# Kernel optimization log

Hardware: AMD Instinct MI355X
Metric: run time of the kernel (lower is better)

## Reference

```python
import jax, jax.numpy as jnp
from jax import lax
import numpy as np

INPUT_SIZE = 128
T = 64
B = 8192
HIDDENS = [32, 16, 8]
FUTURE = 1


def _lstm_layer(x, w_ih, w_hh, b_ih, b_hh):
    """PyTorch-semantics single-layer LSTM, batch_first, zero init state.
    x: [B,T,D]; w_ih: [4H,D]; w_hh: [4H,H]; b_ih,b_hh: [4H]. Gate order i,f,g,o.
    Returns all hidden states [B,T,H]."""
    Bsz = x.shape[0]
    H = w_hh.shape[1]
    # Precompute input contribution for all timesteps in one big GEMM.
    xg = jnp.einsum('btd,gd->btg', x, w_ih) + b_ih + b_hh  # [B,T,4H]
    xg_t = jnp.swapaxes(xg, 0, 1)  # [T,B,4H]

    def step(carry, xt):
        h, c = carry
        gates = xt + h @ w_hh.T  # [B,4H]
        i, f, g, o = jnp.split(gates, 4, axis=-1)
        i = jax.nn.sigmoid(i)
        f = jax.nn.sigmoid(f)
        g = jnp.tanh(g)
        o = jax.nn.sigmoid(o)
        c = f * c + i * g
        h = o * jnp.tanh(c)
        return (h, c), h

    init = (jnp.zeros((Bsz, H), x.dtype), jnp.zeros((Bsz, H), x.dtype))
    _, hs = lax.scan(step, init, xg_t)  # hs: [T,B,H]
    return jnp.swapaxes(hs, 0, 1)


def setup_inputs() -> dict:
    key = jax.random.key(0)
    ks = jax.random.split(key, 16)
    s = 0.1

    def rn(k, shape):
        return jax.random.normal(k, shape, dtype=jnp.float32) * s

    inp = {
        'x': jax.random.normal(ks[0], (B, T, INPUT_SIZE), dtype=jnp.float32),
        'w_ih1': rn(ks[1], (4 * 32, INPUT_SIZE)),
        'w_hh1': rn(ks[2], (4 * 32, 32)),
        'b_ih1': rn(ks[3], (4 * 32,)),
        'b_hh1': rn(ks[4], (4 * 32,)),
        'w_ih2': rn(ks[5], (4 * 16, 32)),
        'w_hh2': rn(ks[6], (4 * 16, 16)),
        'b_ih2': rn(ks[7], (4 * 16,)),
        'b_hh2': rn(ks[8], (4 * 16,)),
        'w_ih3': rn(ks[9], (4 * 8, 16)),
        'w_hh3': rn(ks[10], (4 * 8, 8)),
        'b_ih3': rn(ks[11], (4 * 8,)),
        'b_hh3': rn(ks[12], (4 * 8,)),
        'fc_w': rn(ks[13], (FUTURE, 8)),
        'fc_b': rn(ks[14], (FUTURE,)),
    }
    return inp


def reference(x, w_ih1, w_hh1, b_ih1, b_hh1, w_ih2, w_hh2, b_ih2, b_hh2,
              w_ih3, w_hh3, b_ih3, b_hh3, fc_w, fc_b):
    h = _lstm_layer(x, w_ih1, w_hh1, b_ih1, b_hh1)   # [B,T,32]
    h = _lstm_layer(h, w_ih2, w_hh2, b_ih2, b_hh2)   # [B,T,16]
    h = _lstm_layer(h, w_ih3, w_hh3, b_ih3, b_hh3)   # [B,T,8]
    return h[:, -1, :] @ fc_w.T + fc_b               # [B, FUTURE]
```

## Files before the change

### kernel.cpp

```cpp
#include <hip/hip_runtime.h>
#include <cstddef>
#include <type_traits>


typedef _Float16 h8_t  __attribute__((ext_vector_type(8)));
typedef __fp16   p2_t  __attribute__((ext_vector_type(2)));
typedef float    f4_t  __attribute__((ext_vector_type(4)));

#define T_LEN 64
#define D_IN  128

__device__ __forceinline__ float sig_(float x)  { return 1.0f / (1.0f + __expf(-x)); }
__device__ __forceinline__ float tanh_(float x) { float e = __expf(2.0f * x); return 1.0f - 2.0f / (e + 1.0f); }

__device__ __forceinline__ h8_t zero8h() {
    h8_t r = { (_Float16)0.f,(_Float16)0.f,(_Float16)0.f,(_Float16)0.f,
               (_Float16)0.f,(_Float16)0.f,(_Float16)0.f,(_Float16)0.f };
    return r;
}
__device__ __forceinline__ h8_t cvt8(f4_t lo, f4_t hi) {
    union { h8_t v8; p2_t v2[4]; } u;
    u.v2[0] = __builtin_amdgcn_cvt_pkrtz(lo[0], lo[1]);
    u.v2[1] = __builtin_amdgcn_cvt_pkrtz(lo[2], lo[3]);
    u.v2[2] = __builtin_amdgcn_cvt_pkrtz(hi[0], hi[1]);
    u.v2[3] = __builtin_amdgcn_cvt_pkrtz(hi[2], hi[3]);
    return u.v8;
}
__device__ __forceinline__ h8_t load8f_h(const float* __restrict__ p) {
    f4_t lo = *(const f4_t*)p, hi = *(const f4_t*)(p + 4);
    return cvt8(lo, hi);
}

__global__ __launch_bounds__(256, 2)
void lstm_one(const float* __restrict__ x,
              const float* __restrict__ w_ih1, const float* __restrict__ w_hh1,
              const float* __restrict__ b_ih1, const float* __restrict__ b_hh1,
              const float* __restrict__ w_ih2, const float* __restrict__ w_hh2,
              const float* __restrict__ b_ih2, const float* __restrict__ b_hh2,
              const float* __restrict__ w_ih3, const float* __restrict__ w_hh3,
              const float* __restrict__ b_ih3, const float* __restrict__ b_hh3,
              const float* __restrict__ fc_w, const float* __restrict__ fc_b,
              float* __restrict__ out)
{
    __shared__ __align__(16) _Float16 h1s[2][16][40];
    __shared__ __align__(16) _Float16 h2s[2][16][24];
    __shared__ __align__(16) _Float16 h3s[2][16][8];
    __shared__ __align__(16) _Float16 xs[2][16 * 128];

    const int tid  = threadIdx.x;
    const int lane = tid & 63;
    const int wid  = tid >> 6;
    const int nl = lane & 15, qd = lane >> 4;
    const int n7 = nl & 7;
    const bool lo8 = (nl & 8) == 0;

    h8_t bw1[2][4], bh1[2];
    #pragma unroll
    for (int j = 0; j < 2; ++j) {
        int G = 8 * wid + n7 + 32 * ((nl >> 3) + 2 * j);
        #pragma unroll
        for (int kc = 0; kc < 4; ++kc)
            bw1[j][kc] = load8f_h(w_ih1 + G * 128 + kc * 32 + qd * 8);
        bh1[j] = load8f_h(w_hh1 + G * 32 + qd * 8);
    }
    h8_t bw2[2] = {zero8h(), zero8h()}, bh2[2] = {zero8h(), zero8h()};
    float bs2[4] = {0.f, 0.f, 0.f, 0.f};
    if (wid < 2) {
        #pragma unroll
        for (int j = 0; j < 2; ++j) {
            int G = 32 * j + 16 * (nl >> 3) + 8 * wid + n7;
            bw2[j] = load8f_h(w_ih2 + G * 32 + qd * 8);
            bh2[j] = (qd < 2) ? load8f_h(w_hh2 + G * 16 + qd * 8) : zero8h();
        }
        int u2 = 8 * wid + n7;
        #pragma unroll
        for (int g = 0; g < 4; ++g) bs2[g] = b_ih2[16 * g + u2] + b_hh2[16 * g + u2];
    }
    h8_t b3c[2] = {zero8h(), zero8h()};
    float bs3[4] = {0.f, 0.f, 0.f, 0.f};
    if (wid >= 2) {
        #pragma unroll
        for (int j = 0; j < 2; ++j) {
            int G = 16 * j + 8 * (nl >> 3) + n7;
            b3c[j] = (qd < 2) ? load8f_h(w_ih3 + G * 16 + qd * 8)
                   : (qd == 2) ? load8f_h(w_hh3 + G * 8) : zero8h();
        }
        #pragma unroll
        for (int g = 0; g < 4; ++g) bs3[g] = b_ih3[8 * g + n7] + b_hh3[8 * g + n7];
    }
    float bs1[4];
    {
        int u1 = 8 * wid + n7;
        #pragma unroll
        for (int g = 0; g < 4; ++g) bs1[g] = b_ih1[32 * g + u1] + b_hh1[32 * g + u1];
    }

    for (int i = tid; i < 2 * 16 * 40; i += 256) (&h1s[0][0][0])[i] = (_Float16)0.f;
    for (int i = tid; i < 2 * 16 * 24; i += 256) (&h2s[0][0][0])[i] = (_Float16)0.f;
    for (int i = tid; i < 2 * 16 * 8;  i += 256) (&h3s[0][0][0])[i] = (_Float16)0.f;

    float c1[2] = {0.f, 0.f};
    float c2[2] = {0.f, 0.f};
    float c3    = 0.f;

    const int b0 = blockIdx.x * 16;

    const int xrow = tid >> 4, xcc = tid & 15;
    const float* xg = x + ((size_t)(b0 + xrow) * T_LEN) * D_IN + xcc * 8;
    const int xws = (xrow * 16 + (xcc ^ (xrow & 7))) * 8;

    f4_t xa0 = *(const f4_t*)xg, xa1 = *(const f4_t*)(xg + 4);
    *(h8_t*)&xs[0][xws] = cvt8(xa0, xa1);
    xa0 = *(const f4_t*)(xg + D_IN);
    xa1 = *(const f4_t*)(xg + D_IN + 4);
    __syncthreads();

    auto step = [&](auto d1c, auto d2c, auto d3c, auto pc, int t) {
        constexpr bool DO1 = decltype(d1c)::value;
        constexpr bool DO2 = decltype(d2c)::value;
        constexpr bool DO3 = decltype(d3c)::value;
        constexpr int  P   = decltype(pc)::value;

        h8_t a1p = zero8h();
        if constexpr (DO1 || DO2)
            a1p = *(const h8_t*)&h1s[1 - P][nl][qd * 8];

        if constexpr (DO1) {
            h8_t af[4];
            #pragma unroll
            for (int kc = 0; kc < 4; ++kc)
                af[kc] = *(const h8_t*)&xs[P][(nl * 16 + ((4 * kc + qd) ^ n7)) * 8];

            h8_t xcur = cvt8(xa0, xa1);
            {
                int tn = (t + 2 < T_LEN) ? (t + 2) : (T_LEN - 1);
                const float* xn = xg + (size_t)tn * D_IN;
                xa0 = *(const f4_t*)xn;
                xa1 = *(const f4_t*)(xn + 4);
            }
            *(h8_t*)&xs[1 - P][xws] = xcur;

            f4_t acc[2];
            #pragma unroll
            for (int j = 0; j < 2; ++j) {
                f4_t a_ = {0.f, 0.f, 0.f, 0.f};
                #pragma unroll
                for (int kc = 0; kc < 4; ++kc)
                    a_ = __builtin_amdgcn_mfma_f32_16x16x32_f16(af[kc], bw1[j][kc], a_, 0, 0, 0);
                a_ = __builtin_amdgcn_mfma_f32_16x16x32_f16(a1p, bh1[j], a_, 0, 0, 0);
                acc[j] = a_;
            }
            #pragma unroll
            for (int rr = 0; rr < 2; ++rr) {
                float s0 = lo8 ? acc[0][rr + 2] : acc[0][rr];
                float s1 = lo8 ? acc[1][rr + 2] : acc[1][rr];
                float x0 = __shfl_xor(s0, 8, 64);
                float x1 = __shfl_xor(s1, 8, 64);
                float vi = lo8 ? acc[0][rr] : x0;
                float vf = lo8 ? x0 : acc[0][rr + 2];
                float vg = lo8 ? acc[1][rr] : x1;
                float vo = lo8 ? x1 : acc[1][rr + 2];
                float ig = sig_(vi + bs1[0]);
                float fg = sig_(vf + bs1[1]);
                float gg = tanh_(vg + bs1[2]);
                float og = sig_(vo + bs1[3]);
                float c = fg * c1[rr] + ig * gg; c1[rr] = c;
                float h = og * tanh_(c);
                h1s[P][4 * qd + rr + (lo8 ? 0 : 2)][8 * wid + n7] = (_Float16)h;
            }
        }

        if constexpr (DO2) {
            if (wid < 2) {
                h8_t a2p = zero8h();
                if (qd < 2) a2p = *(const h8_t*)&h2s[P][nl][qd * 8];
                f4_t acc2[2];
                #pragma unroll
                for (int j = 0; j < 2; ++j) {
                    f4_t a_ = {0.f, 0.f, 0.f, 0.f};
                    a_ = __builtin_amdgcn_mfma_f32_16x16x32_f16(a1p, bw2[j], a_, 0, 0, 0);
                    a_ = __builtin_amdgcn_mfma_f32_16x16x32_f16(a2p, bh2[j], a_, 0, 0, 0);
                    acc2[j] = a_;
                }
                #pragma unroll
                for (int rr = 0; rr < 2; ++rr) {
                    float s0 = lo8 ? acc2[0][rr + 2] : acc2[0][rr];
                    float s1 = lo8 ? acc2[1][rr + 2] : acc2[1][rr];
                    float x0 = __shfl_xor(s0, 8, 64);
                    float x1 = __shfl_xor(s1, 8, 64);
                    float vi = lo8 ? acc2[0][rr] : x0;
                    float vf = lo8 ? x0 : acc2[0][rr + 2];
                    float vg = lo8 ? acc2[1][rr] : x1;
                    float vo = lo8 ? x1 : acc2[1][rr + 2];
                    float ig = sig_(vi + bs2[0]);
                    float fg = sig_(vf + bs2[1]);
                    float gg = tanh_(vg + bs2[2]);
                    float og = sig_(vo + bs2[3]);
                    float c = fg * c2[rr] + ig * gg; c2[rr] = c;
                    float h = og * tanh_(c);
                    h2s[1 - P][4 * qd + rr + (lo8 ? 0 : 2)][8 * wid + n7] = (_Float16)h;
                }
            }
        }

        if constexpr (DO3) {
            if (wid >= 2) {
                h8_t a3 = zero8h();
                if (qd < 2)       a3 = *(const h8_t*)&h2s[P][nl][qd * 8];
                else if (qd == 2) a3 = *(const h8_t*)&h3s[1 - P][nl][0];
                f4_t acc3[2];
                #pragma unroll
                for (int j = 0; j < 2; ++j) {
                    f4_t a_ = {0.f, 0.f, 0.f, 0.f};
                    acc3[j] = __builtin_amdgcn_mfma_f32_16x16x32_f16(a3, b3c[j], a_, 0, 0, 0);
                }
                auto l3c = [&](auto rpc) {
                    constexpr int rp = decltype(rpc)::value;
                    float eLo = acc3[0][rp], eHi = acc3[0][rp + 2];
                    float oLo = acc3[1][rp], oHi = acc3[1][rp + 2];
                    float se = lo8 ? eHi : eLo; float xe = __shfl_xor(se, 8, 64);
                    float so = lo8 ? oHi : oLo; float xo = __shfl_xor(so, 8, 64);
                    float vi = lo8 ? eLo : xe;
                    float vf = lo8 ? xe  : eHi;
                    float vg = lo8 ? oLo : xo;
                    float vo = lo8 ? xo  : oHi;
                    float ig = sig_(vi + bs3[0]);
                    float fg = sig_(vf + bs3[1]);
                    float gg = tanh_(vg + bs3[2]);
                    float og = sig_(vo + bs3[3]);
                    float c = fg * c3 + ig * gg; c3 = c;
                    float h = og * tanh_(c);
                    h3s[P][4 * qd + rp + (lo8 ? 0 : 2)][n7] = (_Float16)h;
                };
                if (wid == 2) l3c(std::integral_constant<int, 0>{});
                else          l3c(std::integral_constant<int, 1>{});
            }
        }

        __syncthreads();
    };

    using TT = std::integral_constant<bool, true>;
    using FF = std::integral_constant<bool, false>;
    using P0 = std::integral_constant<int, 0>;
    using P1 = std::integral_constant<int, 1>;

    step(TT{}, FF{}, FF{}, P0{}, 0);
    step(TT{}, TT{}, FF{}, P1{}, 1);
    for (int tb = 1; tb < 32; ++tb) {
        step(TT{}, TT{}, TT{}, P0{}, 2 * tb);
        step(TT{}, TT{}, TT{}, P1{}, 2 * tb + 1);
    }
    step(FF{}, TT{}, TT{}, P0{}, 64);
    step(FF{}, FF{}, TT{}, P1{}, 65);

    if (tid < 16) {
        float a = fc_b[0];
        #pragma unroll
        for (int u = 0; u < 8; ++u)
            a += fc_w[u] * (float)h3s[1][tid][u];
        out[b0 + tid] = a;
    }
}

extern "C" void kernel_launch(void* const* d_in, const int* in_sizes, int n_in,
                              void* d_out, int out_size, void* d_ws, size_t ws_size,
                              hipStream_t stream) {
    (void)in_sizes; (void)n_in; (void)out_size; (void)d_ws; (void)ws_size;
    const float* x     = (const float*)d_in[0];
    const float* w_ih1 = (const float*)d_in[1];
    const float* w_hh1 = (const float*)d_in[2];
    const float* b_ih1 = (const float*)d_in[3];
    const float* b_hh1 = (const float*)d_in[4];
    const float* w_ih2 = (const float*)d_in[5];
    const float* w_hh2 = (const float*)d_in[6];
    const float* b_ih2 = (const float*)d_in[7];
    const float* b_hh2 = (const float*)d_in[8];
    const float* w_ih3 = (const float*)d_in[9];
    const float* w_hh3 = (const float*)d_in[10];
    const float* b_ih3 = (const float*)d_in[11];
    const float* b_hh3 = (const float*)d_in[12];
    const float* fc_w  = (const float*)d_in[13];
    const float* fc_b  = (const float*)d_in[14];

    dim3 grid(512), block(256);
    hipLaunchKernelGGL(lstm_one, grid, block, 0, stream,
                       x, w_ih1, w_hh1, b_ih1, b_hh1,
                       w_ih2, w_hh2, b_ih2, b_hh2,
                       w_ih3, w_hh3, b_ih3, b_hh3,
                       fc_w, fc_b, (float*)d_out);
}
```

Baseline: 411.7 us.

## Double block to 512 threads, splitting LSTM elementwise rows across wave pairs

Launches 8 waves per block instead of 4. Each pair of waves redundantly runs the same MFMAs, but each wave handles only one of the two row halves in the gate nonlinearity, which halves the serial elementwise chain per wave. The x prefetch is now split into 4-float chunks per thread, and the per-step __syncthreads is replaced by an explicit lgkmcnt wait plus s_barrier. The cost is duplicated MFMA work and weight registers, and a barrier across more waves.

```diff
diff --git a/kernel.cpp b/kernel.cpp
--- a/kernel.cpp
+++ b/kernel.cpp
@@ -4,6 +4,7 @@
 
 
 typedef _Float16 h8_t  __attribute__((ext_vector_type(8)));
+typedef _Float16 h4_t  __attribute__((ext_vector_type(4)));
 typedef __fp16   p2_t  __attribute__((ext_vector_type(2)));
 typedef float    f4_t  __attribute__((ext_vector_type(4)));
 
@@ -26,12 +27,23 @@
     u.v2[3] = __builtin_amdgcn_cvt_pkrtz(hi[2], hi[3]);
     return u.v8;
 }
+__device__ __forceinline__ h4_t cvt4(f4_t v) {
+    union { h4_t v4; p2_t v2[2]; } u;
+    u.v2[0] = __builtin_amdgcn_cvt_pkrtz(v[0], v[1]);
+    u.v2[1] = __builtin_amdgcn_cvt_pkrtz(v[2], v[3]);
+    return u.v4;
+}
 __device__ __forceinline__ h8_t load8f_h(const float* __restrict__ p) {
     f4_t lo = *(const f4_t*)p, hi = *(const f4_t*)(p + 4);
     return cvt8(lo, hi);
 }
 
-__global__ __launch_bounds__(256, 2)
+__device__ __forceinline__ void bar_lds() {
+    asm volatile("s_waitcnt lgkmcnt(0)" ::: "memory");
+    __builtin_amdgcn_s_barrier();
+}
+
+__global__ __launch_bounds__(512, 4)
 void lstm_one(const float* __restrict__ x,
               const float* __restrict__ w_ih1, const float* __restrict__ w_hh1,
               const float* __restrict__ b_ih1, const float* __restrict__ b_hh1,
@@ -49,7 +61,9 @@
 
     const int tid  = threadIdx.x;
     const int lane = tid & 63;
-    const int wid  = tid >> 6;
+    const int wid8 = tid >> 6;
+    const int w    = wid8 & 3;
+    const int rsel = wid8 >> 2;
     const int nl = lane & 15, qd = lane >> 4;
     const int n7 = nl & 7;
     const bool lo8 = (nl & 8) == 0;
@@ -57,7 +71,7 @@
     h8_t bw1[2][4], bh1[2];
     #pragma unroll
     for (int j = 0; j < 2; ++j) {
-        int G = 8 * wid + n7 + 32 * ((nl >> 3) + 2 * j);
+        int G = 8 * w + n7 + 32 * ((nl >> 3) + 2 * j);
         #pragma unroll
         for (int kc = 0; kc < 4; ++kc)
             bw1[j][kc] = load8f_h(w_ih1 + G * 128 + kc * 32 + qd * 8);
@@ -65,20 +79,20 @@
     }
     h8_t bw2[2] = {zero8h(), zero8h()}, bh2[2] = {zero8h(), zero8h()};
     float bs2[4] = {0.f, 0.f, 0.f, 0.f};
-    if (wid < 2) {
+    if (w < 2) {
         #pragma unroll
         for (int j = 0; j < 2; ++j) {
-            int G = 32 * j + 16 * (nl >> 3) + 8 * wid + n7;
+            int G = 32 * j + 16 * (nl >> 3) + 8 * w + n7;
             bw2[j] = load8f_h(w_ih2 + G * 32 + qd * 8);
             bh2[j] = (qd < 2) ? load8f_h(w_hh2 + G * 16 + qd * 8) : zero8h();
         }
-        int u2 = 8 * wid + n7;
+        int u2 = 8 * w + n7;
         #pragma unroll
         for (int g = 0; g < 4; ++g) bs2[g] = b_ih2[16 * g + u2] + b_hh2[16 * g + u2];
     }
     h8_t b3c[2] = {zero8h(), zero8h()};
     float bs3[4] = {0.f, 0.f, 0.f, 0.f};
-    if (wid >= 2) {
+    if (wid8 == 2 || wid8 == 3) {
         #pragma unroll
         for (int j = 0; j < 2; ++j) {
             int G = 16 * j + 8 * (nl >> 3) + n7;
@@ -90,29 +104,28 @@
     }
     float bs1[4];
     {
-        int u1 = 8 * wid + n7;
+        int u1 = 8 * w + n7;
         #pragma unroll
         for (int g = 0; g < 4; ++g) bs1[g] = b_ih1[32 * g + u1] + b_hh1[32 * g + u1];
     }
 
-    for (int i = tid; i < 2 * 16 * 40; i += 256) (&h1s[0][0][0])[i] = (_Float16)0.f;
-    for (int i = tid; i < 2 * 16 * 24; i += 256) (&h2s[0][0][0])[i] = (_Float16)0.f;
-    for (int i = tid; i < 2 * 16 * 8;  i += 256) (&h3s[0][0][0])[i] = (_Float16)0.f;
-
-    float c1[2] = {0.f, 0.f};
-    float c2[2] = {0.f, 0.f};
-    float c3    = 0.f;
+    for (int i = tid; i < 2 * 16 * 40; i += 512) (&h1s[0][0][0])[i] = (_Float16)0.f;
+    for (int i = tid; i < 2 * 16 * 24; i += 512) (&h2s[0][0][0])[i] = (_Float16)0.f;
+    for (int i = tid; i < 2 * 16 * 8;  i += 512) (&h3s[0][0][0])[i] = (_Float16)0.f;
+
+    float c1 = 0.f;
+    float c2 = 0.f;
+    float c3 = 0.f;
 
     const int b0 = blockIdx.x * 16;
 
-    const int xrow = tid >> 4, xcc = tid & 15;
-    const float* xg = x + ((size_t)(b0 + xrow) * T_LEN) * D_IN + xcc * 8;
-    const int xws = (xrow * 16 + (xcc ^ (xrow & 7))) * 8;
-
-    f4_t xa0 = *(const f4_t*)xg, xa1 = *(const f4_t*)(xg + 4);
-    *(h8_t*)&xs[0][xws] = cvt8(xa0, xa1);
-    xa0 = *(const f4_t*)(xg + D_IN);
-    xa1 = *(const f4_t*)(xg + D_IN + 4);
+    const int xrow = tid >> 5, xch = (tid >> 1) & 15, xh = tid & 1;
+    const float* xg = x + ((size_t)(b0 + xrow) * T_LEN) * D_IN + xch * 8 + xh * 4;
+    const int xws = (xrow * 16 + (xch ^ (xrow & 7))) * 8 + xh * 4;
+
+    f4_t xa = *(const f4_t*)xg;
+    *(h4_t*)&xs[0][xws] = cvt4(xa);
+    xa = *(const f4_t*)(xg + D_IN);
     __syncthreads();
 
     auto step = [&](auto d1c, auto d2c, auto d3c, auto pc, int t) {
@@ -131,14 +144,12 @@
             for (int kc = 0; kc < 4; ++kc)
                 af[kc] = *(const h8_t*)&xs[P][(nl * 16 + ((4 * kc + qd) ^ n7)) * 8];
 
-            h8_t xcur = cvt8(xa0, xa1);
+            h4_t xcur = cvt4(xa);
             {
                 int tn = (t + 2 < T_LEN) ? (t + 2) : (T_LEN - 1);
-                const float* xn = xg + (size_t)tn * D_IN;
-                xa0 = *(const f4_t*)xn;
-                xa1 = *(const f4_t*)(xn + 4);
+                xa = *(const f4_t*)(xg + tn * D_IN);
             }
-            *(h8_t*)&xs[1 - P][xws] = xcur;
+            *(h4_t*)&xs[1 - P][xws] = xcur;
 
             f4_t acc[2];
             #pragma unroll
@@ -150,8 +161,8 @@
                 a_ = __builtin_amdgcn_mfma_f32_16x16x32_f16(a1p, bh1[j], a_, 0, 0, 0);
                 acc[j] = a_;
             }
-            #pragma unroll
-            for (int rr = 0; rr < 2; ++rr) {
+            auto ew1 = [&](auto rrc) {
+                constexpr int rr = decltype(rrc)::value;
                 float s0 = lo8 ? acc[0][rr + 2] : acc[0][rr];
                 float s1 = lo8 ? acc[1][rr + 2] : acc[1][rr];
                 float x0 = __shfl_xor(s0, 8, 64);
@@ -164,14 +175,16 @@
                 float fg = sig_(vf + bs1[1]);
                 float gg = tanh_(vg + bs1[2]);
                 float og = sig_(vo + bs1[3]);
-                float c = fg * c1[rr] + ig * gg; c1[rr] = c;
+                float c = fg * c1 + ig * gg; c1 = c;
                 float h = og * tanh_(c);
-                h1s[P][4 * qd + rr + (lo8 ? 0 : 2)][8 * wid + n7] = (_Float16)h;
-            }
+                h1s[P][4 * qd + rr + (lo8 ? 0 : 2)][8 * w + n7] = (_Float16)h;
+            };
+            if (rsel == 0) ew1(std::integral_constant<int, 0>{});
+            else           ew1(std::integral_constant<int, 1>{});
         }
 
         if constexpr (DO2) {
-            if (wid < 2) {
+            if (w < 2) {
                 h8_t a2p = zero8h();
                 if (qd < 2) a2p = *(const h8_t*)&h2s[P][nl][qd * 8];
                 f4_t acc2[2];
@@ -182,8 +195,8 @@
                     a_ = __builtin_amdgcn_mfma_f32_16x16x32_f16(a2p, bh2[j], a_, 0, 0, 0);
                     acc2[j] = a_;
                 }
-                #pragma unroll
-                for (int rr = 0; rr < 2; ++rr) {
+                auto ew2 = [&](auto rrc) {
+                    constexpr int rr = decltype(rrc)::value;
                     float s0 = lo8 ? acc2[0][rr + 2] : acc2[0][rr];
                     float s1 = lo8 ? acc2[1][rr + 2] : acc2[1][rr];
                     float x0 = __shfl_xor(s0, 8, 64);
@@ -196,15 +209,17 @@
                     float fg = sig_(vf + bs2[1]);
                     float gg = tanh_(vg + bs2[2]);
                     float og = sig_(vo + bs2[3]);
-                    float c = fg * c2[rr] + ig * gg; c2[rr] = c;
+                    float c = fg * c2 + ig * gg; c2 = c;
                     float h = og * tanh_(c);
-                    h2s[1 - P][4 * qd + rr + (lo8 ? 0 : 2)][8 * wid + n7] = (_Float16)h;
-                }
+                    h2s[1 - P][4 * qd + rr + (lo8 ? 0 : 2)][8 * w + n7] = (_Float16)h;
+                };
+                if (rsel == 0) ew2(std::integral_constant<int, 0>{});
+                else           ew2(std::integral_constant<int, 1>{});
             }
         }
 
         if constexpr (DO3) {
-            if (wid >= 2) {
+            if (wid8 == 2 || wid8 == 3) {
                 h8_t a3 = zero8h();
                 if (qd < 2)       a3 = *(const h8_t*)&h2s[P][nl][qd * 8];
                 else if (qd == 2) a3 = *(const h8_t*)&h3s[1 - P][nl][0];
@@ -232,12 +247,12 @@
                     float h = og * tanh_(c);
                     h3s[P][4 * qd + rp + (lo8 ? 0 : 2)][n7] = (_Float16)h;
                 };
-                if (wid == 2) l3c(std::integral_constant<int, 0>{});
-                else          l3c(std::integral_constant<int, 1>{});
+                if (wid8 == 2) l3c(std::integral_constant<int, 0>{});
+                else           l3c(std::integral_constant<int, 1>{});
             }
         }
 
-        __syncthreads();
+        bar_lds();
     };
 
     using TT = std::integral_constant<bool, true>;
@@ -283,7 +298,7 @@
     const float* fc_w  = (const float*)d_in[13];
     const float* fc_b  = (const float*)d_in[14];
 
-    dim3 grid(512), block(256);
+    dim3 grid(512), block(512);
     hipLaunchKernelGGL(lstm_one, grid, block, 0, stream,
                        x, w_ih1, w_hh1, b_ih1, b_hh1,
                        w_ih2, w_hh2, b_ih2, b_hh2,
```

Measured after the change: 457.9 us. 11.2% more time.
